# Optimization experiments

Measured on AMD Instinct MI355X. Metric: run time of the kernel, lower is better.

## Reference

```python
import jax, jax.numpy as jnp
import numpy as np

B, NIN, L, N, K, NOUT = 4096, 512, 16, 512, 32, 256
TOTAL = NIN + L * N  # 8704 total nodes in the DAG


def setup_inputs() -> dict:
    key = jax.random.key(0)
    ks = jax.random.split(key, 5)
    x = jax.random.normal(ks[0], (B, NIN), jnp.float32)
    W = jax.random.normal(ks[1], (L, N, K), jnp.float32) * 0.2
    b = jax.random.normal(ks[2], (L, N), jnp.float32) * 0.1
    W_out = jax.random.normal(ks[3], (NOUT, K), jnp.float32) * 0.2
    b_out = jax.random.normal(ks[4], (NOUT,), jnp.float32) * 0.1
    rng = np.random.default_rng(0)
    # layer l may only read nodes computed before it (topological validity)
    idx = np.stack([rng.integers(0, NIN + l * N, size=(N, K)) for l in range(L)]).astype(np.int32)
    idx_out = rng.integers(0, TOTAL, size=(NOUT, K)).astype(np.int32)
    return {"x": x, "W": W, "b": b, "W_out": W_out, "b_out": b_out,
            "idx": jnp.asarray(idx), "idx_out": jnp.asarray(idx_out)}


def reference(x, W, b, W_out, b_out, idx, idx_out):
    # buffer of all node activations, filled topologically (out_dict analog)
    buf0 = jnp.zeros((B, TOTAL), x.dtype).at[:, :NIN].set(x)

    def step(carry, layer):
        buf, l = carry
        li, lW, lb = layer
        gathered = buf[:, li]  # [B, N, K] irregular gather of predecessor outputs
        out = jax.nn.sigmoid(jnp.einsum('bnk,nk->bn', gathered, lW) + lb)  # per-node tiny linear + sigmoid
        buf = jax.lax.dynamic_update_slice(buf, out, (0, NIN + l * N))
        return (buf, l + 1), None

    (buf, _), _ = jax.lax.scan(step, (buf0, jnp.int32(0)), (idx, W, b))
    g = buf[:, idx_out]  # [B, NOUT, K]
    return jax.nn.sigmoid(jnp.einsum('bok,ok->bo', g, W_out) + b_out)
```

## Files before the change

kernel.cpp:

```cpp
#include <hip/hip_runtime.h>
#include <hip/hip_fp16.h>
#include <math.h>

#define B     4096
#define NIN   512
#define L     16
#define N     512
#define K     32
#define NOUT  256
#define HID   (L * N)
#define TOTAL (NIN + L * N)
#define BROWS 4
#define BLOCK 512

typedef __attribute__((ext_vector_type(2))) _Float16 hv2;
typedef __attribute__((ext_vector_type(8))) _Float16 h8;
typedef __attribute__((ext_vector_type(8))) unsigned short u16x8;

struct alignas(8) hh { hv2 lo, hi; };

__device__ __forceinline__ float sigmoidf_fast(float z) {
    return 1.0f / (1.0f + __expf(-z));
}

__global__ void repack_kernel(const float* __restrict__ W,
                              const int*   __restrict__ idx,
                              const float* __restrict__ W_out,
                              const int*   __restrict__ idx_out,
                              _Float16* __restrict__ wh,
                              unsigned short* __restrict__ i16,
                              _Float16* __restrict__ who,
                              unsigned short* __restrict__ io16)
{
    const int n = blockIdx.x * 64 + threadIdx.x;
    const int* ip; const float* wp; _Float16* wo; unsigned short* io; int scale;
    if (n < HID) {
        ip = idx + (size_t)n * K;      wp = W + (size_t)n * K;
        wo = wh + (size_t)n * K;       io = i16 + (size_t)n * K;   scale = 3;
    } else if (n < HID + NOUT) {
        const int m = n - HID;
        ip = idx_out + (size_t)m * K;  wp = W_out + (size_t)m * K;
        wo = who + (size_t)m * K;      io = io16 + (size_t)m * K;  scale = 0;
    } else {
        return;
    }
    const int rot = n & 15;

    int ci[K]; float cw[K];
    {
        const int4*   ip4 = (const int4*)ip;
        const float4* wp4 = (const float4*)wp;
#pragma unroll
        for (int q = 0; q < 8; ++q) {
            const int4   a = ip4[q];
            const float4 f = wp4[q];
            ci[q * 4 + 0] = a.x; ci[q * 4 + 1] = a.y;
            ci[q * 4 + 2] = a.z; ci[q * 4 + 3] = a.w;
            cw[q * 4 + 0] = f.x; cw[q * 4 + 1] = f.y;
            cw[q * 4 + 2] = f.z; cw[q * 4 + 3] = f.w;
        }
    }

    unsigned long long r0 = 0, r1 = 0;
    int sl[K];
    unsigned used = 0;
#pragma unroll
    for (int j = 0; j < K; ++j) {
        const int key = ci[j] & 15;
        const int sh  = (key & 7) << 3;
        int rank;
        if (key < 8) { rank = (int)((r0 >> sh) & 0xff); r0 += 1ull << sh; }
        else         { rank = (int)((r1 >> sh) & 0xff); r1 += 1ull << sh; }
        if (rank < 2) {
            const int s = ((key - rot) & 15) + (rank << 4);
            sl[j] = s; used |= 1u << s;
        } else {
            sl[j] = -1;
        }
    }
#pragma unroll
    for (int j = 0; j < K; ++j) {
        int s = sl[j];
        if (s < 0) { s = (int)__builtin_ctz(~used); used |= 1u << s; }
        io[s] = (unsigned short)(ci[j] << scale);
        wo[s] = (_Float16)cw[j];
    }
}

#define GATHERS(CI, V, SH)                                                    \
    _Pragma("unroll")                                                         \
    for (int j = 0; j < 8; ++j) {                                             \
        const int c = ((int)(CI)[j]) << (SH);                                 \
        (V)[j] = *(const hh*)((const char*)buf + c);                          \
    }

#define FMA8(V, W8, ACC)                                                      \
    {                                                                         \
        hv2 aL = {(_Float16)0.f, (_Float16)0.f};                              \
        hv2 aH = {(_Float16)0.f, (_Float16)0.f};                              \
        _Pragma("unroll")                                                     \
        for (int j = 0; j < 8; ++j) {                                         \
            hv2 wt2; wt2.x = (W8)[j]; wt2.y = (W8)[j];                        \
            aL = __builtin_elementwise_fma((V)[j].lo, wt2, aL);               \
            aH = __builtin_elementwise_fma((V)[j].hi, wt2, aH);               \
        }                                                                     \
        (ACC).x += (float)aL.x;  (ACC).y += (float)aL.y;                      \
        (ACC).z += (float)aH.x;  (ACC).w += (float)aH.y;                      \
    }

#define LAYER(IDXQ, LI)                                                       \
    {                                                                         \
        const h8* wp = (const h8*)(wh + ((size_t)(LI) * N + t) * K);          \
        const h8 w0 = wp[0], w1 = wp[1], w2 = wp[2], w3 = wp[3];              \
        const float bb = bias[(LI) * N + t];                                  \
        hh v0[8], v1[8], v2[8], v3[8];                                        \
        GATHERS(IDXQ[0], v0, 0)                                               \
        GATHERS(IDXQ[1], v1, 0)                                               \
        GATHERS(IDXQ[2], v2, 0)                                               \
        float4 acc = make_float4(0.f, 0.f, 0.f, 0.f);                         \
        FMA8(v0, w0, acc)                                                     \
        GATHERS(IDXQ[3], v3, 0)                                               \
        FMA8(v1, w1, acc)                                                     \
        FMA8(v2, w2, acc)                                                     \
        FMA8(v3, w3, acc)                                                     \
        hh o;                                                                 \
        o.lo.x = (_Float16)sigmoidf_fast(acc.x + bb);                         \
        o.lo.y = (_Float16)sigmoidf_fast(acc.y + bb);                         \
        o.hi.x = (_Float16)sigmoidf_fast(acc.z + bb);                         \
        o.hi.y = (_Float16)sigmoidf_fast(acc.w + bb);                         \
        buf[NIN + (LI) * N + t] = o;                                          \
    }

__global__ __launch_bounds__(BLOCK, 4)
void ffnet_kernel(const float* __restrict__ x,
                  const float* __restrict__ bias,
                  const float* __restrict__ bias_out,
                  const _Float16*       __restrict__ wh,
                  const unsigned short* __restrict__ i16,
                  const _Float16*       __restrict__ who,
                  const unsigned short* __restrict__ io16,
                  float* __restrict__ out)
{
    __shared__ hh buf[TOTAL];

    const int t  = threadIdx.x;
    const int r0 = blockIdx.x * BROWS;

    {
        hh v;
        v.lo.x = (_Float16)x[(size_t)(r0 + 0) * NIN + t];
        v.lo.y = (_Float16)x[(size_t)(r0 + 1) * NIN + t];
        v.hi.x = (_Float16)x[(size_t)(r0 + 2) * NIN + t];
        v.hi.y = (_Float16)x[(size_t)(r0 + 3) * NIN + t];
        buf[t] = v;
    }

    u16x8 ia[4], ib[4];
    {
        const u16x8* ip = (const u16x8*)(i16 + (size_t)t * K);
        ia[0] = ip[0]; ia[1] = ip[1]; ia[2] = ip[2]; ia[3] = ip[3];
    }
    __syncthreads();

    for (int l = 0; l < L; l += 2) {
        {
            const u16x8* np = (const u16x8*)(i16 + ((size_t)(l + 1) * N + t) * K);
            ib[0] = np[0]; ib[1] = np[1]; ib[2] = np[2]; ib[3] = np[3];
        }
        LAYER(ia, l)
        __syncthreads();

        if (l + 2 < L) {
            const u16x8* np = (const u16x8*)(i16 + ((size_t)(l + 2) * N + t) * K);
            ia[0] = np[0]; ia[1] = np[1]; ia[2] = np[2]; ia[3] = np[3];
        } else if (t < NOUT) {
            const u16x8* np = (const u16x8*)(io16 + (size_t)t * K);
            ia[0] = np[0]; ia[1] = np[1]; ia[2] = np[2]; ia[3] = np[3];
        }
        LAYER(ib, l + 1)
        __syncthreads();
    }

    if (t < NOUT) {
        const h8* wp = (const h8*)(who + (size_t)t * K);
        const h8 w0 = wp[0], w1 = wp[1], w2 = wp[2], w3 = wp[3];
        const float bb = bias_out[t];

        hh v0[8], v1[8], v2[8], v3[8];
        GATHERS(ia[0], v0, 3)
        GATHERS(ia[1], v1, 3)
        GATHERS(ia[2], v2, 3)
        float4 acc = make_float4(0.f, 0.f, 0.f, 0.f);
        FMA8(v0, w0, acc)
        GATHERS(ia[3], v3, 3)
        FMA8(v1, w1, acc)
        FMA8(v2, w2, acc)
        FMA8(v3, w3, acc)

        out[(size_t)(r0 + 0) * NOUT + t] = sigmoidf_fast(acc.x + bb);
        out[(size_t)(r0 + 1) * NOUT + t] = sigmoidf_fast(acc.y + bb);
        out[(size_t)(r0 + 2) * NOUT + t] = sigmoidf_fast(acc.z + bb);
        out[(size_t)(r0 + 3) * NOUT + t] = sigmoidf_fast(acc.w + bb);
    }
}

extern "C" void kernel_launch(void* const* d_in, const int* in_sizes, int n_in,
                              void* d_out, int out_size, void* d_ws, size_t ws_size,
                              hipStream_t stream) {
    const float* x     = (const float*)d_in[0];
    const float* W     = (const float*)d_in[1];
    const float* b     = (const float*)d_in[2];
    const float* W_out = (const float*)d_in[3];
    const float* b_out = (const float*)d_in[4];
    const int*   idx   = (const int*)d_in[5];
    const int*   idx_o = (const int*)d_in[6];
    float* out = (float*)d_out;

    char* ws = (char*)d_ws;
    _Float16*       wh   = (_Float16*)      (ws);
    unsigned short* i16  = (unsigned short*)(ws + 524288);
    _Float16*       who  = (_Float16*)      (ws + 1048576);
    unsigned short* io16 = (unsigned short*)(ws + 1048576 + 16384);

    const int nneur = HID + NOUT;
    repack_kernel<<<dim3((nneur + 63) / 64), dim3(64), 0, stream>>>(
        W, idx, W_out, idx_o, wh, i16, who, io16);

    ffnet_kernel<<<dim3(B / BROWS), dim3(BLOCK), 0, stream>>>(
        x, b, b_out, wh, i16, who, io16, out);
}
```

Measured before the change: 145.2 us.

## Assign overflow gather slots using wavefront ballot to reduce bank conflicts

The repack kernel previously put overflow indices (beyond two per low-4-bit key) into the first free slot. Now each lane runs a 32-step ballot loop and, for each free slot, picks an overflow index whose bank key is not already taken by the other lanes in its 16-lane group at that slot position. The aim is fewer bank or channel conflicts in the main kernel's gathers, at the cost of a heavier one-time repack. The guard for n beyond the last neuron is dropped, which relies on nneur being a multiple of 64.

```diff
diff --git a/kernel.cpp b/kernel.cpp
--- a/kernel.cpp
+++ b/kernel.cpp
@@ -32,17 +32,16 @@
                               _Float16* __restrict__ who,
                               unsigned short* __restrict__ io16)
 {
-    const int n = blockIdx.x * 64 + threadIdx.x;
+    const int lane = threadIdx.x;
+    const int n = blockIdx.x * 64 + lane;
     const int* ip; const float* wp; _Float16* wo; unsigned short* io; int scale;
     if (n < HID) {
         ip = idx + (size_t)n * K;      wp = W + (size_t)n * K;
         wo = wh + (size_t)n * K;       io = i16 + (size_t)n * K;   scale = 3;
-    } else if (n < HID + NOUT) {
+    } else {
         const int m = n - HID;
         ip = idx_out + (size_t)m * K;  wp = W_out + (size_t)m * K;
         wo = who + (size_t)m * K;      io = io16 + (size_t)m * K;  scale = 0;
-    } else {
-        return;
     }
     const int rot = n & 15;
 
@@ -61,13 +60,15 @@
         }
     }
 
-    unsigned long long r0 = 0, r1 = 0;
+    unsigned long long r0 = 0, r1 = 0, kp0 = 0, kp1 = 0;
     int sl[K];
     unsigned used = 0;
 #pragma unroll
     for (int j = 0; j < K; ++j) {
         const int key = ci[j] & 15;
-        const int sh  = (key & 7) << 3;
+        if (j < 16) kp0 |= (unsigned long long)key << (4 * j);
+        else        kp1 |= (unsigned long long)key << (4 * (j - 16));
+        const int sh = (key & 7) << 3;
         int rank;
         if (key < 8) { rank = (int)((r0 >> sh) & 0xff); r0 += 1ull << sh; }
         else         { rank = (int)((r1 >> sh) & 0xff); r1 += 1ull << sh; }
@@ -78,10 +79,49 @@
             sl[j] = -1;
         }
     }
+    const unsigned hm = ~used;
+    unsigned sm = 0;
+#pragma unroll
+    for (int j = 0; j < K; ++j) if (sl[j] < 0) sm |= 1u << j;
+
+    unsigned long long spl0 = 0, spl1 = 0, spl2 = 0, spl3 = 0;
+    for (int s = 0; s < 32; ++s) {
+        const bool holed = (hm >> s) & 1u;
+        const unsigned long long bal = __ballot(holed);
+        const unsigned slice = (unsigned)((bal >> (lane & 48)) & 0xFFFFull);
+        const unsigned shf = (unsigned)(s & 15);
+        const unsigned avail =
+            ((slice << shf) | (slice >> ((16u - shf) & 15u))) & 0xFFFFu;
+        if (holed) {
+            unsigned m = sm;
+            int b = -1;
+            while (m) {
+                const int bb = (int)__builtin_ctz(m);
+                const unsigned long long sel = (bb & 16) ? kp1 : kp0;
+                const int k = (int)((sel >> ((bb & 15) << 2)) & 15);
+                if ((avail >> k) & 1u) { b = bb; break; }
+                m &= m - 1;
+            }
+            if (b < 0) b = (int)__builtin_ctz(sm);
+            sm &= ~(1u << b);
+            const unsigned long long w = (unsigned long long)s << ((b & 7) << 3);
+            const int hi = b >> 3;
+            spl0 = (hi == 0) ? (spl0 | w) : spl0;
+            spl1 = (hi == 1) ? (spl1 | w) : spl1;
+            spl2 = (hi == 2) ? (spl2 | w) : spl2;
+            spl3 = (hi == 3) ? (spl3 | w) : spl3;
+        }
+    }
+
 #pragma unroll
     for (int j = 0; j < K; ++j) {
         int s = sl[j];
-        if (s < 0) { s = (int)__builtin_ctz(~used); used |= 1u << s; }
+        if (s < 0) {
+            const unsigned long long sp =
+                (j >> 3) == 0 ? spl0 : (j >> 3) == 1 ? spl1
+              : (j >> 3) == 2 ? spl2 : spl3;
+            s = (int)((sp >> ((j & 7) << 3)) & 0x3F);
+        }
         io[s] = (unsigned short)(ci[j] << scale);
         wo[s] = (_Float16)cw[j];
     }
@@ -223,7 +263,7 @@
     unsigned short* io16 = (unsigned short*)(ws + 1048576 + 16384);
 
     const int nneur = HID + NOUT;
-    repack_kernel<<<dim3((nneur + 63) / 64), dim3(64), 0, stream>>>(
+    repack_kernel<<<dim3(nneur / 64), dim3(64), 0, stream>>>(
         W, idx, W_out, idx_o, wh, i16, who, io16);
 
     ffnet_kernel<<<dim3(B / BROWS), dim3(BLOCK), 0, stream>>>(
```

Result: slower. 168.8 us (+16.3%).
